# Kernel optimization log

Hardware: AMD Instinct MI355X
Metric: run time of the kernel (lower is better)

The kernel has to match this reference:

```python
import jax, jax.numpy as jnp
import numpy as np

# NF4 codebook (QLoRA): 16 quantile values of a standard normal, normalized to [-1, 1]
NF4_TABLE = jnp.array([
    -1.0, -0.6961928009986877, -0.5250730514526367, -0.39491748809814453,
    -0.28444138169288635, -0.18477343022823334, -0.09105003625154495, 0.0,
    0.07958029955625534, 0.16093020141124725, 0.24611230194568634,
    0.33791524171829224, 0.44070982933044434, 0.5626170039176941,
    0.7229568362236328, 1.0], dtype=jnp.float32)

IN_DIM = 4096
OUT_DIM = 4096
RANK = 16
ALPHA = 32.0
BLOCK = 64  # NF4 quantization block size along the flattened weight


def setup_inputs() -> dict:
    key = jax.random.key(0)
    k1, k2, k3, k4, k5 = jax.random.split(key, 5)
    x = jax.random.normal(k1, (4, 2048, IN_DIM), dtype=jnp.float32)
    # 4-bit codes into NF4_TABLE, stored unpacked as int32
    w_codes = jax.random.randint(k2, (OUT_DIM, IN_DIM), 0, 16, dtype=jnp.int32)
    # per-block absmax scales (positive)
    w_scales = jax.random.uniform(k3, (OUT_DIM, IN_DIM // BLOCK), dtype=jnp.float32) * 0.02 + 1e-3
    # lora_a: kaiming-uniform-ish scale; lora_b: nonzero for testability (original inits to zeros)
    lora_a = jax.random.normal(k4, (RANK, IN_DIM), dtype=jnp.float32) * (1.0 / np.sqrt(IN_DIM))
    lora_b = jax.random.normal(k5, (OUT_DIM, RANK), dtype=jnp.float32) * 0.01
    return {"x": x, "w_codes": w_codes, "w_scales": w_scales, "lora_a": lora_a, "lora_b": lora_b}


def _dequant_nf4(w_codes, w_scales):
    # codes [O, I] -> dequantized weight [O, I]
    w = NF4_TABLE[w_codes]                                   # [O, I]
    w = w.reshape(OUT_DIM, IN_DIM // BLOCK, BLOCK) * w_scales[:, :, None]
    return w.reshape(OUT_DIM, IN_DIM)


def reference(x, w_codes, w_scales, lora_a, lora_b):
    # base: frozen NF4 linear (dequantize then matmul), no bias
    w = _dequant_nf4(w_codes, w_scales)                      # [O, I]
    base = jnp.einsum('bsi,oi->bso', x, w)                   # [B, S, O]
    # LoRA path: dropout p=0.0 -> identity; scale alpha / rank
    ax = jnp.einsum('bsi,ri->bsr', x, lora_a)                # [B, S, r]
    lora = jnp.einsum('bsr,or->bso', ax, lora_b)             # [B, S, O]
    return base + (ALPHA / RANK) * lora
```

## Files before the change

kernel.cpp:

```cpp
#include <hip/hip_runtime.h>
#include <hip/hip_bf16.h>


#define IN_DIM  4096
#define OUT_DIM 4096
#define RANK    16
#define M_TOK   8192
#define LORA_SCALE 2.0f

typedef __bf16 bf16_t;
typedef bf16_t bf16x8 __attribute__((ext_vector_type(8)));
typedef float  f32x4  __attribute__((ext_vector_type(4)));

__device__ __constant__ float NF4_TAB[16] = {
    -1.0f, -0.6961928009986877f, -0.5250730514526367f, -0.39491748809814453f,
    -0.28444138169288635f, -0.18477343022823334f, -0.09105003625154495f, 0.0f,
    0.07958029955625534f, 0.16093020141124725f, 0.24611230194568634f,
    0.33791524171829224f, 0.44070982933044434f, 0.5626170039176941f,
    0.7229568362236328f, 1.0f};

__global__ __launch_bounds__(256) void prep_all(
    const float* __restrict__ x,
    const int* __restrict__ codes, const float* __restrict__ scales,
    const float* __restrict__ la, const float* __restrict__ lb,
    bf16_t* __restrict__ W, bf16_t* __restrict__ xb)
{
    const int tid = threadIdx.x;
    if (blockIdx.x < 1024) {
        __shared__ float nf4s[16];
        __shared__ float lbs[4][16];
        const int o0 = blockIdx.x * 4;
        if (tid < 64) lbs[tid >> 4][tid & 15] = lb[(o0 + (tid >> 4)) * RANK + (tid & 15)] * LORA_SCALE;
        else if (tid < 80) nf4s[tid - 64] = NF4_TAB[tid - 64];
        __syncthreads();

        #pragma unroll
        for (int it = 0; it < 2; ++it) {
            const int i0 = (it * 256 + tid) * 8;
            float w[4][8];
            #pragma unroll
            for (int oo = 0; oo < 4; ++oo) {
                const size_t base = (size_t)(o0 + oo) * IN_DIM + i0;
                int4 c0 = *(const int4*)(codes + base);
                int4 c1 = *(const int4*)(codes + base + 4);
                const float sc = scales[(o0 + oo) * (IN_DIM / 64) + (i0 >> 6)];
                w[oo][0] = nf4s[c0.x] * sc; w[oo][1] = nf4s[c0.y] * sc;
                w[oo][2] = nf4s[c0.z] * sc; w[oo][3] = nf4s[c0.w] * sc;
                w[oo][4] = nf4s[c1.x] * sc; w[oo][5] = nf4s[c1.y] * sc;
                w[oo][6] = nf4s[c1.z] * sc; w[oo][7] = nf4s[c1.w] * sc;
            }
            #pragma unroll
            for (int r = 0; r < RANK; ++r) {
                float4 a0 = *(const float4*)(la + r * IN_DIM + i0);
                float4 a1 = *(const float4*)(la + r * IN_DIM + i0 + 4);
                #pragma unroll
                for (int oo = 0; oo < 4; ++oo) {
                    const float b = lbs[oo][r];
                    w[oo][0] += b * a0.x; w[oo][1] += b * a0.y;
                    w[oo][2] += b * a0.z; w[oo][3] += b * a0.w;
                    w[oo][4] += b * a1.x; w[oo][5] += b * a1.y;
                    w[oo][6] += b * a1.z; w[oo][7] += b * a1.w;
                }
            }
            #pragma unroll
            for (int oo = 0; oo < 4; ++oo) {
                bf16x8 v;
                #pragma unroll
                for (int j = 0; j < 8; ++j) v[j] = (bf16_t)w[oo][j];
                *(bf16x8*)(W + (size_t)(o0 + oo) * IN_DIM + i0) = v;
            }
        }
    } else {
        const int bid = blockIdx.x - 1024;
        const int n8 = (M_TOK * IN_DIM) / 8;
        const int stride = 2048 * 256;
        for (int i = bid * 256 + tid; i < n8; i += stride) {
            const size_t e = (size_t)i * 8;
            float4 a = *(const float4*)(x + e);
            float4 b = *(const float4*)(x + e + 4);
            bf16x8 v;
            v[0] = (bf16_t)a.x; v[1] = (bf16_t)a.y; v[2] = (bf16_t)a.z; v[3] = (bf16_t)a.w;
            v[4] = (bf16_t)b.x; v[5] = (bf16_t)b.y; v[6] = (bf16_t)b.z; v[7] = (bf16_t)b.w;
            *(bf16x8*)(xb + e) = v;
        }
    }
}

__global__ __launch_bounds__(512, 2) void gemm_bt(
    const bf16_t* __restrict__ A, const bf16_t* __restrict__ B,
    float* __restrict__ C)
{
    __shared__ __align__(128) char lds[131072];

    const int tid  = threadIdx.x;
    const int wave = tid >> 6;
    const int lane = tid & 63;

    const int flat = blockIdx.y * gridDim.x + blockIdx.x;
    const int swz  = (flat & 7) * 64 + (flat >> 3);
    const int bx = swz & 15;
    const int by = swz >> 4;
    const int m0 = by * 256;
    const int n0 = bx * 256;

    const int wr = wave >> 2;
    const int wc = wave & 3;

    f32x4 acc[8][4];
    #pragma unroll
    for (int i = 0; i < 8; ++i)
        #pragma unroll
        for (int j = 0; j < 4; ++j) acc[i][j] = (f32x4)0.0f;

    const int frow = lane & 15;
    const int fch  = lane >> 4;
    const int fxor = (fch ^ ((frow >> 1) & 3)) << 4;
    const int aoff = (wr * 128 + frow) * 64 + fxor;
    const int boff = (wc * 64  + frow) * 64 + fxor;

    const int d0 = tid * 16, d1 = 8192 + tid * 16;
    const int sr0 = d0 >> 6, sr1 = d1 >> 6;
    const int sg0 = ((d0 >> 4) & 3) ^ ((sr0 >> 1) & 3);
    const int sg1 = ((d1 >> 4) & 3) ^ ((sr1 >> 1) & 3);
    const char* gA = (const char*)A;
    const char* gB = (const char*)B;

    bf16x8 fAe[8], fAo[8], fBe[2], fBo[2];

#define RD_A2(FA, SL, KH, J0) do {                                             \
    const char* b_ = lds + (SL) * 65536 + (KH) * 16384;                        \
    FA[(J0)]     = *(const bf16x8*)(b_ + aoff + (J0) * 1024);                  \
    FA[(J0) + 1] = *(const bf16x8*)(b_ + aoff + ((J0) + 1) * 1024);            \
} while (0)

#define RD_B(FB, SL, KH, NH) do {                                              \
    const char* b_ = lds + (SL) * 65536 + 32768 + (KH) * 16384;                \
    FB[0] = *(const bf16x8*)(b_ + boff + (NH) * 2048);                         \
    FB[1] = *(const bf16x8*)(b_ + boff + (NH) * 2048 + 1024);                  \
} while (0)

#define STG1(OPI, KH_, SL, T) do {                                             \
    const char* g_  = (OPI) ? gB : gA;                                         \
    const int   r0_ = (OPI) ? n0 : m0;                                         \
    const size_t ko_ = (size_t)(T) * 128 + (KH_) * 64;                         \
    const char* s0_ = g_ + (size_t)(r0_ + sr0) * 8192 + ko_ + (sg0 << 4);      \
    const char* s1_ = g_ + (size_t)(r0_ + sr1) * 8192 + ko_ + (sg1 << 4);      \
    char* db_ = lds + (SL) * 65536 + (OPI) * 32768 + (KH_) * 16384 + wave * 1024; \
    __builtin_amdgcn_global_load_lds(                                          \
        (const __attribute__((address_space(1))) void*)s0_,                    \
        (__attribute__((address_space(3))) void*)db_, 16, 0, 0);               \
    __builtin_amdgcn_global_load_lds(                                          \
        (const __attribute__((address_space(1))) void*)s1_,                    \
        (__attribute__((address_space(3))) void*)(db_ + 8192), 16, 0, 0);      \
} while (0)

#define MM4(FA, F0, FB, BI, NH) do {                                           \
    _Pragma("unroll")                                                          \
    for (int f_ = 0; f_ < 4; ++f_)                                             \
        acc[(F0) + f_][(NH) * 2 + (BI)] =                                      \
            __builtin_amdgcn_mfma_f32_16x16x32_bf16(                           \
                FA[(F0) + f_], FB[BI], acc[(F0) + f_][(NH) * 2 + (BI)], 0, 0, 0); \
} while (0)

#define PHASE(SOP, SKH, SSL, ST, CHK, FA, FB, NH, RD1, RD2, RD3) do {          \
    __builtin_amdgcn_s_setprio(1);                                             \
    MM4(FA, 0, FB, 0, NH);                                                     \
    RD1;                                                                       \
    MM4(FA, 0, FB, 1, NH);                                                     \
    STG1(SOP, SKH, SSL, ST);                                                   \
    MM4(FA, 4, FB, 0, NH);                                                     \
    RD2;                                                                       \
    MM4(FA, 4, FB, 1, NH);                                                     \
    RD3;                                                                       \
    __builtin_amdgcn_s_setprio(0);                                             \
    if (CHK) { asm volatile("s_waitcnt vmcnt(6)" ::: "memory"); }              \
    __builtin_amdgcn_s_barrier();                                              \
} while (0)

    STG1(0, 0, 0, 0); STG1(1, 0, 0, 0); STG1(0, 1, 0, 0); STG1(1, 1, 0, 0);
    STG1(0, 0, 1, 1); STG1(1, 0, 1, 1); STG1(0, 1, 1, 1);
    asm volatile("s_waitcnt vmcnt(6)" ::: "memory");
    __builtin_amdgcn_s_barrier();
    RD_A2(fAe, 0, 0, 0); RD_A2(fAe, 0, 0, 2);
    RD_A2(fAe, 0, 0, 4); RD_A2(fAe, 0, 0, 6);
    RD_B(fBe, 0, 0, 0);

    for (int i = 0; i < 32; ++i) {
        const int tY  = 2 * i + 1;
        const int tS0 = (2 * i + 2) & 63;
        const int tS1 = (2 * i + 3) & 63;
        PHASE(1, 1, 1, tY,  0, fAe, fBe, 0,
              RD_A2(fAo, 0, 1, 0), RD_A2(fAo, 0, 1, 2), RD_B(fBo, 0, 0, 1));
        PHASE(0, 0, 0, tS0, 1, fAe, fBo, 1,
              RD_A2(fAo, 0, 1, 4), RD_A2(fAo, 0, 1, 6), RD_B(fBe, 0, 1, 0));
        PHASE(1, 0, 0, tS0, 0, fAo, fBe, 0,
              RD_A2(fAe, 1, 0, 0), RD_A2(fAe, 1, 0, 2), RD_B(fBo, 0, 1, 1));
        PHASE(0, 1, 0, tS0, 1, fAo, fBo, 1,
              RD_A2(fAe, 1, 0, 4), RD_A2(fAe, 1, 0, 6), RD_B(fBe, 1, 0, 0));
        PHASE(1, 1, 0, tS0, 0, fAe, fBe, 0,
              RD_A2(fAo, 1, 1, 0), RD_A2(fAo, 1, 1, 2), RD_B(fBo, 1, 0, 1));
        PHASE(0, 0, 1, tS1, 1, fAe, fBo, 1,
              RD_A2(fAo, 1, 1, 4), RD_A2(fAo, 1, 1, 6), RD_B(fBe, 1, 1, 0));
        PHASE(1, 0, 1, tS1, 0, fAo, fBe, 0,
              RD_A2(fAe, 0, 0, 0), RD_A2(fAe, 0, 0, 2), RD_B(fBo, 1, 1, 1));
        PHASE(0, 1, 1, tS1, 1, fAo, fBo, 1,
              RD_A2(fAe, 0, 0, 4), RD_A2(fAe, 0, 0, 6), RD_B(fBe, 0, 0, 0));
    }

    const int crow = (lane >> 4) * 4;
    const int ccol = lane & 15;
    #pragma unroll
    for (int i = 0; i < 8; ++i) {
        #pragma unroll
        for (int j = 0; j < 4; ++j) {
            const int mb = m0 + wr * 128 + i * 16 + crow;
            const int nb = n0 + wc * 64 + j * 16 + ccol;
            #pragma unroll
            for (int r = 0; r < 4; ++r)
                C[(size_t)(mb + r) * OUT_DIM + nb] = acc[i][j][r];
        }
    }
#undef RD_A2
#undef RD_B
#undef STG1
#undef MM4
#undef PHASE
}

extern "C" void kernel_launch(void* const* d_in, const int* in_sizes, int n_in,
                              void* d_out, int out_size, void* d_ws, size_t ws_size,
                              hipStream_t stream) {
    const float* x      = (const float*)d_in[0];
    const int*   codes  = (const int*)d_in[1];
    const float* scales = (const float*)d_in[2];
    const float* la     = (const float*)d_in[3];
    const float* lb     = (const float*)d_in[4];
    float* out = (float*)d_out;

    bf16_t* W  = (bf16_t*)d_ws;
    bf16_t* xb = (bf16_t*)((char*)d_ws + (size_t)OUT_DIM * IN_DIM * 2);

    prep_all<<<1024 + 2048, 256, 0, stream>>>(x, codes, scales, la, lb, W, xb);

    dim3 grid(OUT_DIM / 256, M_TOK / 256);
    gemm_bt<<<grid, 512, 0, stream>>>(xb, W, out);
}
```

Measured before the change: 281.2 us.

## Restructure GEMM main loop into four regions with fewer barriers

Replaces the eight-phase software pipeline, which placed a barrier after each phase, with four larger regions. Each region issues two global-to-LDS stage loads, runs 32 MFMAs across both B halves, and interleaves the next A/B fragment reads. Waits now use vmcnt(4) with one fewer load in flight in the prologue. The goal is to halve barrier and wait overhead per K-step and give the MFMA stream longer uninterrupted runs. The cost is a shallower prefetch depth and more fragment registers live at once.

```diff
diff --git a/kernel.cpp b/kernel.cpp
--- a/kernel.cpp
+++ b/kernel.cpp
@@ -162,49 +162,45 @@
                 FA[(F0) + f_], FB[BI], acc[(F0) + f_][(NH) * 2 + (BI)], 0, 0, 0); \
 } while (0)
 
-#define PHASE(SOP, SKH, SSL, ST, CHK, FA, FB, NH, RD1, RD2, RD3) do {          \
+#define REGION(FA, FAN, RSL, RKH, A_OP, A_KH, A_SL, A_T, B_OP, B_KH, B_SL, B_T) do { \
+    STG1(A_OP, A_KH, A_SL, A_T);                                               \
     __builtin_amdgcn_s_setprio(1);                                             \
-    MM4(FA, 0, FB, 0, NH);                                                     \
-    RD1;                                                                       \
-    MM4(FA, 0, FB, 1, NH);                                                     \
-    STG1(SOP, SKH, SSL, ST);                                                   \
-    MM4(FA, 4, FB, 0, NH);                                                     \
-    RD2;                                                                       \
-    MM4(FA, 4, FB, 1, NH);                                                     \
-    RD3;                                                                       \
+    MM4(FA, 0, fBe, 0, 0);                                                     \
+    MM4(FA, 4, fBe, 0, 0);                                                     \
+    RD_A2(FAN, RSL, RKH, 0);                                                   \
+    MM4(FA, 0, fBe, 1, 0);                                                     \
+    MM4(FA, 4, fBe, 1, 0);                                                     \
+    RD_B(fBe, RSL, RKH, 0);                                                    \
+    STG1(B_OP, B_KH, B_SL, B_T);                                               \
+    MM4(FA, 0, fBo, 0, 1);                                                     \
+    RD_A2(FAN, RSL, RKH, 2);                                                   \
+    MM4(FA, 4, fBo, 0, 1);                                                     \
+    RD_A2(FAN, RSL, RKH, 4);                                                   \
+    MM4(FA, 0, fBo, 1, 1);                                                     \
+    RD_A2(FAN, RSL, RKH, 6);                                                   \
+    MM4(FA, 4, fBo, 1, 1);                                                     \
+    RD_B(fBo, RSL, RKH, 1);                                                    \
     __builtin_amdgcn_s_setprio(0);                                             \
-    if (CHK) { asm volatile("s_waitcnt vmcnt(6)" ::: "memory"); }              \
+    asm volatile("s_waitcnt vmcnt(4)" ::: "memory");                           \
     __builtin_amdgcn_s_barrier();                                              \
 } while (0)
 
     STG1(0, 0, 0, 0); STG1(1, 0, 0, 0); STG1(0, 1, 0, 0); STG1(1, 1, 0, 0);
-    STG1(0, 0, 1, 1); STG1(1, 0, 1, 1); STG1(0, 1, 1, 1);
-    asm volatile("s_waitcnt vmcnt(6)" ::: "memory");
+    STG1(0, 0, 1, 1); STG1(1, 0, 1, 1);
+    asm volatile("s_waitcnt vmcnt(4)" ::: "memory");
     __builtin_amdgcn_s_barrier();
     RD_A2(fAe, 0, 0, 0); RD_A2(fAe, 0, 0, 2);
     RD_A2(fAe, 0, 0, 4); RD_A2(fAe, 0, 0, 6);
-    RD_B(fBe, 0, 0, 0);
+    RD_B(fBe, 0, 0, 0);  RD_B(fBo, 0, 0, 1);
 
     for (int i = 0; i < 32; ++i) {
         const int tY  = 2 * i + 1;
         const int tS0 = (2 * i + 2) & 63;
         const int tS1 = (2 * i + 3) & 63;
-        PHASE(1, 1, 1, tY,  0, fAe, fBe, 0,
-              RD_A2(fAo, 0, 1, 0), RD_A2(fAo, 0, 1, 2), RD_B(fBo, 0, 0, 1));
-        PHASE(0, 0, 0, tS0, 1, fAe, fBo, 1,
-              RD_A2(fAo, 0, 1, 4), RD_A2(fAo, 0, 1, 6), RD_B(fBe, 0, 1, 0));
-        PHASE(1, 0, 0, tS0, 0, fAo, fBe, 0,
-              RD_A2(fAe, 1, 0, 0), RD_A2(fAe, 1, 0, 2), RD_B(fBo, 0, 1, 1));
-        PHASE(0, 1, 0, tS0, 1, fAo, fBo, 1,
-              RD_A2(fAe, 1, 0, 4), RD_A2(fAe, 1, 0, 6), RD_B(fBe, 1, 0, 0));
-        PHASE(1, 1, 0, tS0, 0, fAe, fBe, 0,
-              RD_A2(fAo, 1, 1, 0), RD_A2(fAo, 1, 1, 2), RD_B(fBo, 1, 0, 1));
-        PHASE(0, 0, 1, tS1, 1, fAe, fBo, 1,
-              RD_A2(fAo, 1, 1, 4), RD_A2(fAo, 1, 1, 6), RD_B(fBe, 1, 1, 0));
-        PHASE(1, 0, 1, tS1, 0, fAo, fBe, 0,
-              RD_A2(fAe, 0, 0, 0), RD_A2(fAe, 0, 0, 2), RD_B(fBo, 1, 1, 1));
-        PHASE(0, 1, 1, tS1, 1, fAo, fBo, 1,
-              RD_A2(fAe, 0, 0, 4), RD_A2(fAe, 0, 0, 6), RD_B(fBe, 0, 0, 0));
+        REGION(fAe, fAo, 0, 1,  0, 1, 1, tY,   1, 1, 1, tY);
+        REGION(fAo, fAe, 1, 0,  0, 0, 0, tS0,  1, 0, 0, tS0);
+        REGION(fAe, fAo, 1, 1,  0, 1, 0, tS0,  1, 1, 0, tS0);
+        REGION(fAo, fAe, 0, 0,  0, 0, 1, tS1,  1, 0, 1, tS1);
     }
 
     const int crow = (lane >> 4) * 4;
@@ -224,7 +220,7 @@
 #undef RD_B
 #undef STG1
 #undef MM4
-#undef PHASE
+#undef REGION
 }
 
 extern "C" void kernel_launch(void* const* d_in, const int* in_sizes, int n_in,
```

Result: slower. 286.9 us (+2.0%).
